# Performance work log

Measured on AMD Instinct MI355X. Metric: run time of the kernel, lower is better.

## Reference

```python
import jax, jax.numpy as jnp
import numpy as np

N, SD, VD, ED, E, NG, NA, NB = 512, 256, 128, 128, 262144, 16, 16, 5


def _lin_init(key, fan_in, fan_out):
    # torch.nn.Linear default: U(-1/sqrt(fan_in), 1/sqrt(fan_in)); stored as (in, out)
    lim = 1.0 / np.sqrt(fan_in)
    return jax.random.uniform(key, (fan_in, fan_out), jnp.float32, -lim, lim)


def setup_inputs() -> dict:
    key = jax.random.key(0)
    ks = jax.random.split(key, 20)
    s = jax.random.normal(ks[0], (N, SD), jnp.float32)
    v = jax.random.normal(ks[1], (N, 3, VD), jnp.float32)
    p = jax.random.normal(ks[2], (N, 3), jnp.float32)
    e = jax.random.normal(ks[3], (E, ED), jnp.float32)
    batch = jnp.sort(jax.random.randint(ks[4], (N,), 0, NG))
    edge_index_global = jax.random.randint(ks[5], (2, E), 0, N)
    W_sm = _lin_init(ks[6], SD, SD); b_sm = jnp.zeros((SD,), jnp.float32)
    W_bm = _lin_init(ks[7], ED, SD); b_bm = jnp.zeros((SD,), jnp.float32)
    W_b0 = _lin_init(ks[8], SD + 1, SD); b_b0 = jnp.zeros((SD,), jnp.float32)
    W_b1 = _lin_init(ks[9], SD, NB); b_b1 = jnp.zeros((NB,), jnp.float32)
    W_c = _lin_init(ks[10], VD, 1)  # no bias
    W_a = _lin_init(ks[11], SD, NA); b_a = jnp.zeros((NA,), jnp.float32)
    return {"s": s, "v": v, "p": p, "e": e, "batch": batch,
            "edge_index_global": edge_index_global,
            "W_sm": W_sm, "b_sm": b_sm, "W_bm": W_bm, "b_bm": b_bm,
            "W_b0": W_b0, "b_b0": b_b0, "W_b1": W_b1, "b_b1": b_b1,
            "W_c": W_c, "W_a": W_a, "b_a": b_a}


def reference(s, v, p, e, batch, edge_index_global,
              W_sm, b_sm, W_bm, b_bm, W_b0, b_b0, W_b1, b_b1, W_c, W_a, b_a):
    # shared_mapping: Linear + SiLU
    s = jax.nn.silu(s @ W_sm + b_sm)                      # [N, SD]
    coords_pred = (v @ W_c)[..., 0]                       # [N, 3]
    atoms_pred = s @ W_a + b_a                            # [N, NA]
    j, i = edge_index_global[0], edge_index_global[1]
    n = s.shape[0]
    # coords_param == 'data': coords = p + pred, then per-graph mean centering
    coords_pred = p + coords_pred
    seg_sum = jax.ops.segment_sum(coords_pred, batch, num_segments=NG)
    counts = jax.ops.segment_sum(jnp.ones((n, 1), coords_pred.dtype), batch, num_segments=NG)
    mean = seg_sum / jnp.maximum(counts, 1.0)
    coords_pred = coords_pred - mean[batch]
    # squared pairwise distance per edge
    d = jnp.sum((coords_pred[i] - coords_pred[j]) ** 2, axis=-1, keepdims=True)  # [E, 1]
    # sparse -> dense -> sparse symmetrization of edge features (as in the source)
    e_dense = jnp.zeros((n, n, e.shape[-1]), e.dtype).at[j, i].set(e)
    e_dense = 0.5 * (e_dense + jnp.transpose(e_dense, (1, 0, 2)))
    e_sym = e_dense[j, i]                                 # [E, ED]
    f = s[i] + s[j] + (e_sym @ W_bm + b_bm)               # [E, SD]
    edge = jnp.concatenate([f, d], axis=-1)               # [E, SD+1]
    bonds_pred = jax.nn.silu(edge @ W_b0 + b_b0) @ W_b1 + b_b1  # [E, NB]
    return coords_pred, atoms_pred, bonds_pred
```

## Files before the change

### kernel.cpp

```cpp
#include <hip/hip_runtime.h>
#include <math.h>

#define N_NODES 512
#define SD_ 256
#define VD_ 128
#define ED_ 128
#define NE_ 262144
#define NG_ 16
#define NA_ 16
#define NB_ 5
#define MAXP 131328

typedef __attribute__((ext_vector_type(8))) short bf16x8;
typedef __attribute__((ext_vector_type(4))) float f32x4;

__device__ __forceinline__ float silu_f(float x) { return x / (1.0f + expf(-x)); }
__device__ __forceinline__ float silu_fast(float x) {
    return x * __builtin_amdgcn_rcpf(1.0f + __builtin_amdgcn_exp2f(x * -1.44269504f));
}
__device__ __forceinline__ unsigned short f2bf(float x) {
    unsigned int u = __float_as_uint(x);
    return (unsigned short)((u + 0x7fffu + ((u >> 16) & 1u)) >> 16);
}
__device__ __forceinline__ float bf2f(unsigned short h) {
    return __uint_as_float(((unsigned int)h) << 16);
}
__device__ __forceinline__ unsigned int cvt_pk_bf16(float lo, float hi) {
    unsigned int r;
    asm("v_cvt_pk_bf16_f32 %0, %1, %2" : "=v"(r) : "v"(lo), "v"(hi));
    return r;
}

__device__ __forceinline__ void pack_one(
    const float* __restrict__ W, unsigned short* __restrict__ out, int nkb, int idx)
{
    int l = idx & 63;
    int kb = (idx >> 6) % nkb;
    int mtg = idx / (64 * nkb);
    int m = mtg * 16 + (l & 15);
    int k0 = kb * 32 + (l >> 4) * 8;
    bf16x8 pack;
    #pragma unroll
    for (int i = 0; i < 8; ++i) pack[i] = (short)f2bf(W[(size_t)(k0 + i) * SD_ + m]);
    *(bf16x8*)(out + (size_t)idx * 8) = pack;
}

__global__ __launch_bounds__(256) void prep_a(
    const int* __restrict__ ei, int* __restrict__ emap,
    const float* __restrict__ W_bm, const float* __restrict__ W_b0,
    unsigned short* __restrict__ WfA_bm, unsigned short* __restrict__ WfA_b0,
    const float* __restrict__ s, const float* __restrict__ v, const float* __restrict__ p,
    const float* __restrict__ W_sm, const float* __restrict__ b_sm,
    const float* __restrict__ W_a, const float* __restrict__ b_a,
    const float* __restrict__ W_c,
    unsigned short* __restrict__ s2b, float* __restrict__ cpred, float* __restrict__ atoms_out)
{
    __shared__ float srow[8][SD_];
    __shared__ float s2row[8][SD_];
    const int bid = blockIdx.x;
    const int tid = threadIdx.x;

    if (bid < 1024) {
        int k = bid * 256 + tid;
        int j = ei[k], i = ei[NE_ + k];
        atomicMax(&emap[j * N_NODES + i], k);
        return;
    }
    if (bid < 1072) {
        int idx = (bid - 1024) * 256 + tid;
        if (idx < 4096)  pack_one(W_bm, WfA_bm, 4, idx);
        else             pack_one(W_b0, WfA_b0, 8, idx - 4096);
        return;
    }
    if (bid < 1136) {
        const int n0 = (bid - 1072) * 8;
        #pragma unroll
        for (int n = 0; n < 8; ++n) srow[n][tid] = s[(size_t)(n0 + n) * SD_ + tid];
        __syncthreads();
        float acc[8];
        {
            float bb = b_sm[tid];
            #pragma unroll
            for (int n = 0; n < 8; ++n) acc[n] = bb;
        }
        #pragma unroll 4
        for (int c = 0; c < SD_; ++c) {
            float wv = W_sm[(size_t)c * SD_ + tid];
            #pragma unroll
            for (int n = 0; n < 8; ++n) acc[n] = fmaf(srow[n][c], wv, acc[n]);
        }
        #pragma unroll
        for (int n = 0; n < 8; ++n) {
            float sv = silu_f(acc[n]);
            s2b[(size_t)(n0 + n) * SD_ + tid] = f2bf(sv);
            s2row[n][tid] = sv;
        }
        __syncthreads();
        if (tid < 128) {
            int n = tid >> 4, a = tid & 15;
            float x = b_a[a];
            #pragma unroll 8
            for (int c = 0; c < SD_; ++c) x = fmaf(s2row[n][c], W_a[(size_t)c * NA_ + a], x);
            atoms_out[(size_t)(n0 + n) * NA_ + a] = x;
        }
        return;
    }
    for (int o = tid; o < N_NODES * 3; o += 256) {
        float x = p[o];
        const float* vr = v + (size_t)o * VD_;
        #pragma unroll 8
        for (int c = 0; c < VD_; ++c) x = fmaf(vr[c], W_c[c], x);
        cpred[o] = x;
    }
}

__global__ __launch_bounds__(512) void prep_b(
    const float* __restrict__ cpred, const int* __restrict__ batch,
    float* __restrict__ coords_ws, float* __restrict__ coords_out,
    const int* __restrict__ emap, int* __restrict__ counter,
    int* __restrict__ pairslot, int4* __restrict__ worklist)
{
    __shared__ float cl[N_NODES * 3];
    __shared__ int   bl[N_NODES];
    __shared__ float meanv[NG_ * 3];
    const int tid = threadIdx.x;

    if (blockIdx.x == 0) {
        bl[tid] = batch[tid];
        #pragma unroll
        for (int dd = 0; dd < 3; ++dd) cl[tid * 3 + dd] = cpred[tid * 3 + dd];
        __syncthreads();
        if (tid < NG_ * 3) {
            int g = tid / 3, dd = tid % 3;
            float sum = 0.f; int cnt = 0;
            for (int n = 0; n < N_NODES; ++n) {
                if (bl[n] == g) { sum += cl[n * 3 + dd]; cnt++; }
            }
            meanv[tid] = sum / (float)(cnt > 0 ? cnt : 1);
        }
        __syncthreads();
        int g = bl[tid];
        #pragma unroll
        for (int dd = 0; dd < 3; ++dd) {
            float val = cl[tid * 3 + dd] - meanv[g * 3 + dd];
            coords_ws[tid * 3 + dd]  = val;
            coords_out[tid * 3 + dd] = val;
        }
        return;
    }
    int idx = (blockIdx.x - 1) * 512 + tid;
    int a = idx >> 9, b = idx & (N_NODES - 1);
    if (a > b) return;
    int k1 = emap[(a << 9) | b];
    int k2 = emap[(b << 9) | a];
    if (k1 >= 0 || k2 >= 0) {
        int slot = atomicAdd(counter, 1);
        pairslot[(a << 9) | b] = slot;
        pairslot[(b << 9) | a] = slot;
        worklist[slot] = make_int4(a, b, k1, k2);
    }
}

__global__ __launch_bounds__(256) void bonds_scatter(
    const int* __restrict__ ei, const int* __restrict__ pairslot,
    const float* __restrict__ repval, float* __restrict__ bonds_out)
{
    int k = blockIdx.x * 256 + threadIdx.x;
    int j = ei[k], i = ei[NE_ + k];
    int slot = pairslot[(j << 9) | i];
    const float* rp = repval + (size_t)slot * NB_;
    #pragma unroll
    for (int b = 0; b < NB_; ++b)
        bonds_out[(size_t)k * NB_ + b] = rp[b];
}

__global__ __launch_bounds__(512) void edge_mfma(
    const float* __restrict__ e, const int4* __restrict__ worklist,
    const int* __restrict__ counter, const float* __restrict__ coords,
    const float* __restrict__ zrow, const unsigned short* __restrict__ s2b,
    const unsigned short* __restrict__ WfA_bm, const unsigned short* __restrict__ WfA_b0,
    const float* __restrict__ W_b1,
    const float* __restrict__ b_bm, const float* __restrict__ W_b0_last,
    const float* __restrict__ b_b0, const float* __restrict__ b_b1,
    float* __restrict__ repval)
{
    const int blk = blockIdx.x;
    const int cnt = counter[0];
    if (blk * 64 >= cnt) return;

    __shared__ __align__(16) char smem0[64 * 128 * 2];
    __shared__ __align__(16) unsigned short fd_lds[64 * 256];
    __shared__ unsigned short wb1t[NB_ * 256];
    __shared__ float dw[64];
    __shared__ int li_s[64], lj_s[64];

    unsigned short* esym_lds   = (unsigned short*)smem0;
    float*          bonds_part = (float*)smem0;

    const int tid = threadIdx.x;
    const int l   = tid & 63;
    const int w   = tid >> 6;
    const int eLo = l & 15;
    const int hi  = l >> 4;

    if (tid < 256) {
        const int eL = l;
        const int q  = w;
        int widx = min(blk * 64 + eL, cnt - 1);
        int4 wk = worklist[widx];
        const float* r1 = (wk.z >= 0) ? (e + (size_t)wk.z * ED_) : zrow;
        const float* r2 = (wk.w >= 0) ? (e + (size_t)wk.w * ED_) : zrow;
        const float4* p1 = (const float4*)(r1 + q * 32);
        const float4* p2 = (const float4*)(r2 + q * 32);
        float4 va[8], vb[8];
        #pragma unroll
        for (int t = 0; t < 8; ++t) va[t] = p1[t];
        #pragma unroll
        for (int t = 0; t < 8; ++t) vb[t] = p2[t];
        #pragma unroll
        for (int t = 0; t < 8; ++t) {
            va[t].x += vb[t].x; va[t].y += vb[t].y;
            va[t].z += vb[t].z; va[t].w += vb[t].w;
        }
        int ntB = eL >> 4, eLoB = eL & 15;
        #pragma unroll
        for (int h2 = 0; h2 < 4; ++h2) {
            float4 x0 = va[h2 * 2], x1 = va[h2 * 2 + 1];
            uint4 c;
            c.x = cvt_pk_bf16(0.5f * x0.x, 0.5f * x0.y);
            c.y = cvt_pk_bf16(0.5f * x0.z, 0.5f * x0.w);
            c.z = cvt_pk_bf16(0.5f * x1.x, 0.5f * x1.y);
            c.w = cvt_pk_bf16(0.5f * x1.z, 0.5f * x1.w);
            int chunk = (ntB * 4 + q) * 64 + h2 * 16 + eLoB;
            *(uint4*)(&esym_lds[chunk * 8]) = c;
        }
    } else {
        int t = tid - 256;
        #pragma unroll
        for (int b = 0; b < NB_; ++b)
            wb1t[b * 256 + t] = f2bf(W_b1[(size_t)t * NB_ + b]);
        if (t < 64) {
            int widx = min(blk * 64 + t, cnt - 1);
            int4 wk = worklist[widx];
            li_s[t] = wk.x; lj_s[t] = wk.y;
            float dx = coords[wk.x * 3 + 0] - coords[wk.y * 3 + 0];
            float dy = coords[wk.x * 3 + 1] - coords[wk.y * 3 + 1];
            float dz = coords[wk.x * 3 + 2] - coords[wk.y * 3 + 2];
            dw[t] = dx * dx + dy * dy + dz * dz;
        }
    }

    bf16x8 a1p[2];
    #pragma unroll
    for (int mt = 0; mt < 2; ++mt)
        a1p[mt] = *(const bf16x8*)(WfA_bm + ((size_t)(((w * 2 + mt) * 4 + 0) * 64 + l) * 8));

    __syncthreads();

    f32x4 acc[2][4];
    #pragma unroll
    for (int mt = 0; mt < 2; ++mt)
        #pragma unroll
        for (int nt = 0; nt < 4; ++nt) acc[mt][nt] = (f32x4){0.f, 0.f, 0.f, 0.f};

    #pragma unroll
    for (int kb = 0; kb < 4; ++kb) {
        bf16x8 af[2], bfg[4];
        #pragma unroll
        for (int mt = 0; mt < 2; ++mt)
            af[mt] = (kb == 0) ? a1p[mt]
                   : *(const bf16x8*)(WfA_bm + ((size_t)(((w * 2 + mt) * 4 + kb) * 64 + l) * 8));
        #pragma unroll
        for (int nt = 0; nt < 4; ++nt)
            bfg[nt] = *(const bf16x8*)(&esym_lds[(size_t)((nt * 4 + kb) * 64 + l) * 8]);
        __builtin_amdgcn_s_setprio(1);
        #pragma unroll
        for (int mt = 0; mt < 2; ++mt)
            #pragma unroll
            for (int nt = 0; nt < 4; ++nt)
                acc[mt][nt] = __builtin_amdgcn_mfma_f32_16x16x32_bf16(af[mt], bfg[nt], acc[mt][nt], 0, 0, 0);
        __builtin_amdgcn_s_setprio(0);
    }

    bf16x8 a2p[2];
    #pragma unroll
    for (int mt = 0; mt < 2; ++mt)
        a2p[mt] = *(const bf16x8*)(WfA_b0 + ((size_t)(((w * 2 + mt) * 8 + 0) * 64 + l) * 8));

    #pragma unroll
    for (int mt = 0; mt < 2; ++mt) {
        int m0 = w * 32 + mt * 16 + hi * 4;
        float4 bb = *(const float4*)(b_bm + m0);
        #pragma unroll
        for (int nt = 0; nt < 4; ++nt) {
            int edge = nt * 16 + eLo;
            int ni = li_s[edge], nj = lj_s[edge];
            ushort4 si = *(const ushort4*)(s2b + (size_t)ni * SD_ + m0);
            ushort4 sj = *(const ushort4*)(s2b + (size_t)nj * SD_ + m0);
            f32x4 r = acc[mt][nt];
            float f0 = r[0] + bf2f(si.x) + bf2f(sj.x) + bb.x;
            float f1 = r[1] + bf2f(si.y) + bf2f(sj.y) + bb.y;
            float f2 = r[2] + bf2f(si.z) + bf2f(sj.z) + bb.z;
            float f3 = r[3] + bf2f(si.w) + bf2f(sj.w) + bb.w;
            uint2 pk;
            pk.x = cvt_pk_bf16(f0, f1);
            pk.y = cvt_pk_bf16(f2, f3);
            int c16 = m0 >> 3;
            int byteo = (edge << 9) + ((c16 ^ (edge & 7)) << 4) + ((m0 & 7) << 1);
            *(uint2*)((char*)fd_lds + byteo) = pk;
        }
    }
    __syncthreads();

    #pragma unroll
    for (int mt = 0; mt < 2; ++mt) {
        int m0 = w * 32 + mt * 16 + hi * 4;
        float4 b0 = *(const float4*)(b_b0 + m0);
        float4 w2 = *(const float4*)(W_b0_last + m0);
        #pragma unroll
        for (int nt = 0; nt < 4; ++nt) {
            float dd = dw[nt * 16 + eLo];
            acc[mt][nt] = (f32x4){fmaf(dd, w2.x, b0.x), fmaf(dd, w2.y, b0.y),
                                  fmaf(dd, w2.z, b0.z), fmaf(dd, w2.w, b0.w)};
        }
    }
    #pragma unroll
    for (int kb = 0; kb < 8; ++kb) {
        bf16x8 af[2], bfg[4];
        #pragma unroll
        for (int mt = 0; mt < 2; ++mt)
            af[mt] = (kb == 0) ? a2p[mt]
                   : *(const bf16x8*)(WfA_b0 + ((size_t)(((w * 2 + mt) * 8 + kb) * 64 + l) * 8));
        #pragma unroll
        for (int nt = 0; nt < 4; ++nt) {
            int edge = nt * 16 + eLo;
            int c16 = (kb << 2) + hi;
            int byteo = (edge << 9) + ((c16 ^ (edge & 7)) << 4);
            bfg[nt] = *(const bf16x8*)((const char*)fd_lds + byteo);
        }
        __builtin_amdgcn_s_setprio(1);
        #pragma unroll
        for (int mt = 0; mt < 2; ++mt)
            #pragma unroll
            for (int nt = 0; nt < 4; ++nt)
                acc[mt][nt] = __builtin_amdgcn_mfma_f32_16x16x32_bf16(af[mt], bfg[nt], acc[mt][nt], 0, 0, 0);
        __builtin_amdgcn_s_setprio(0);
    }

    float pb[4][NB_];
    #pragma unroll
    for (int nt = 0; nt < 4; ++nt)
        #pragma unroll
        for (int b = 0; b < NB_; ++b) pb[nt][b] = 0.f;
    #pragma unroll
    for (int mt = 0; mt < 2; ++mt) {
        int m0 = w * 32 + mt * 16 + hi * 4;
        ushort4 wv[NB_];
        #pragma unroll
        for (int b = 0; b < NB_; ++b)
            wv[b] = *(const ushort4*)(wb1t + b * 256 + m0);
        #pragma unroll
        for (int nt = 0; nt < 4; ++nt) {
            f32x4 r = acc[mt][nt];
            float h0 = silu_fast(r[0]);
            float h1 = silu_fast(r[1]);
            float h2 = silu_fast(r[2]);
            float h3 = silu_fast(r[3]);
            #pragma unroll
            for (int b = 0; b < NB_; ++b) {
                float t = fmaf(h0, bf2f(wv[b].x), fmaf(h1, bf2f(wv[b].y),
                          fmaf(h2, bf2f(wv[b].z), h3 * bf2f(wv[b].w))));
                pb[nt][b] += t;
            }
        }
    }
    #pragma unroll
    for (int off = 16; off <= 32; off <<= 1)
        #pragma unroll
        for (int nt = 0; nt < 4; ++nt)
            #pragma unroll
            for (int b = 0; b < NB_; ++b)
                pb[nt][b] += __shfl_xor(pb[nt][b], off);

    __syncthreads();
    if (hi == 0) {
        #pragma unroll
        for (int nt = 0; nt < 4; ++nt)
            #pragma unroll
            for (int b = 0; b < NB_; ++b)
                bonds_part[(size_t)(w * 64 + nt * 16 + eLo) * NB_ + b] = pb[nt][b];
    }
    __syncthreads();

    for (int idx = tid; idx < 64 * NB_; idx += 512) {
        int edge = idx / NB_, b = idx % NB_;
        float s8 = 0.f;
        #pragma unroll
        for (int pp = 0; pp < 8; ++pp)
            s8 += bonds_part[(size_t)(pp * 64 + edge) * NB_ + b];
        repval[(size_t)(blk * 64 + edge) * NB_ + b] = s8 + b_b1[b];
    }
}

extern "C" void kernel_launch(void* const* d_in, const int* in_sizes, int n_in,
                              void* d_out, int out_size, void* d_ws, size_t ws_size,
                              hipStream_t stream)
{
    const float* s    = (const float*)d_in[0];
    const float* v    = (const float*)d_in[1];
    const float* p    = (const float*)d_in[2];
    const float* e    = (const float*)d_in[3];
    const int*   batch= (const int*)d_in[4];
    const int*   ei   = (const int*)d_in[5];
    const float* W_sm = (const float*)d_in[6];
    const float* b_sm = (const float*)d_in[7];
    const float* W_bm = (const float*)d_in[8];
    const float* b_bm = (const float*)d_in[9];
    const float* W_b0 = (const float*)d_in[10];
    const float* b_b0 = (const float*)d_in[11];
    const float* W_b1 = (const float*)d_in[12];
    const float* b_b1 = (const float*)d_in[13];
    const float* W_c  = (const float*)d_in[14];
    const float* W_a  = (const float*)d_in[15];
    const float* b_a  = (const float*)d_in[16];

    float* out = (float*)d_out;
    float* coords_out = out;
    float* atoms_out  = out + 1536;
    float* bonds_out  = out + 1536 + 8192;

    char* ws = (char*)d_ws;
    int*            emap    = (int*)ws;
    unsigned short* s2b     = (unsigned short*)(ws + 0x100000);
    unsigned short* WfA_bm  = (unsigned short*)(ws + 0x140000);
    unsigned short* WfA_b0  = (unsigned short*)(ws + 0x150000);
    float*          cpred   = (float*)(ws + 0x170000);
    float*          coords  = (float*)(ws + 0x172000);
    int*            counter = (int*)(ws + 0x175000);
    float*          zrow    = (float*)(ws + 0x175100);
    int*            pairslot= (int*)(ws + 0x180000);
    int4*           worklist= (int4*)(ws + 0x280000);
    float*          repval  = (float*)(ws + 0x4B0000);

    hipMemsetAsync(emap, 0xFF, N_NODES * N_NODES * sizeof(int), stream);
    hipMemsetAsync(ws + 0x175000, 0, 0x300, stream);

    prep_a<<<1137, 256, 0, stream>>>(ei, emap, W_bm, W_b0, WfA_bm, WfA_b0,
                                     s, v, p, W_sm, b_sm, W_a, b_a, W_c,
                                     s2b, cpred, atoms_out);
    prep_b<<<513, 512, 0, stream>>>(cpred, batch, coords, coords_out,
                                    emap, counter, pairslot, worklist);

    edge_mfma<<<(MAXP + 63) / 64, 512, 0, stream>>>(e, worklist, counter, coords, zrow, s2b,
                                                    WfA_bm, WfA_b0, W_b1,
                                                    b_bm, W_b0 + 256 * SD_, b_b0, b_b1,
                                                    repval);
    bonds_scatter<<<NE_ / 256, 256, 0, stream>>>(ei, pairslot, repval, bonds_out);
}
```

Measured before the change: 152.6 us.

## Spread node MLP over more blocks, fold memset into prep, flatten bond scatter

The shared-mapping node MLP now runs 2 nodes per block across 256 blocks instead of 8 nodes per block across 64, which raises parallelism at the cost of more W_sm re-reads. The counter/zrow memset is removed and the reset moves into the prep_a tail block, saving one API op. bonds_scatter now uses one thread per output element so stores coalesce, at the cost of recomputing the pairslot lookup five times per edge. edge_mfma prefetches all four W_bm A-fragments before the sync, which adds register pressure.

```diff
diff --git a/kernel.cpp b/kernel.cpp
--- a/kernel.cpp
+++ b/kernel.cpp
@@ -53,10 +53,11 @@
     const float* __restrict__ W_sm, const float* __restrict__ b_sm,
     const float* __restrict__ W_a, const float* __restrict__ b_a,
     const float* __restrict__ W_c,
-    unsigned short* __restrict__ s2b, float* __restrict__ cpred, float* __restrict__ atoms_out)
-{
-    __shared__ float srow[8][SD_];
-    __shared__ float s2row[8][SD_];
+    unsigned short* __restrict__ s2b, float* __restrict__ cpred, float* __restrict__ atoms_out,
+    int* __restrict__ counter, float* __restrict__ zrow)
+{
+    __shared__ float srow[2][SD_];
+    __shared__ float s2row[2][SD_];
     const int bid = blockIdx.x;
     const int tid = threadIdx.x;
 
@@ -72,31 +73,30 @@
         else             pack_one(W_b0, WfA_b0, 8, idx - 4096);
         return;
     }
-    if (bid < 1136) {
-        const int n0 = (bid - 1072) * 8;
-        #pragma unroll
-        for (int n = 0; n < 8; ++n) srow[n][tid] = s[(size_t)(n0 + n) * SD_ + tid];
+    if (bid < 1328) {
+        const int n0 = (bid - 1072) * 2;
+        #pragma unroll
+        for (int n = 0; n < 2; ++n) srow[n][tid] = s[(size_t)(n0 + n) * SD_ + tid];
         __syncthreads();
-        float acc[8];
+        float acc[2];
         {
             float bb = b_sm[tid];
-            #pragma unroll
-            for (int n = 0; n < 8; ++n) acc[n] = bb;
-        }
-        #pragma unroll 4
+            acc[0] = bb; acc[1] = bb;
+        }
+        #pragma unroll 8
         for (int c = 0; c < SD_; ++c) {
             float wv = W_sm[(size_t)c * SD_ + tid];
-            #pragma unroll
-            for (int n = 0; n < 8; ++n) acc[n] = fmaf(srow[n][c], wv, acc[n]);
-        }
-        #pragma unroll
-        for (int n = 0; n < 8; ++n) {
+            acc[0] = fmaf(srow[0][c], wv, acc[0]);
+            acc[1] = fmaf(srow[1][c], wv, acc[1]);
+        }
+        #pragma unroll
+        for (int n = 0; n < 2; ++n) {
             float sv = silu_f(acc[n]);
             s2b[(size_t)(n0 + n) * SD_ + tid] = f2bf(sv);
             s2row[n][tid] = sv;
         }
         __syncthreads();
-        if (tid < 128) {
+        if (tid < 32) {
             int n = tid >> 4, a = tid & 15;
             float x = b_a[a];
             #pragma unroll 8
@@ -105,6 +105,8 @@
         }
         return;
     }
+    if (tid == 0) counter[0] = 0;
+    if (tid < ED_) zrow[tid] = 0.0f;
     for (int o = tid; o < N_NODES * 3; o += 256) {
         float x = p[o];
         const float* vr = v + (size_t)o * VD_;
@@ -163,15 +165,15 @@
 
 __global__ __launch_bounds__(256) void bonds_scatter(
     const int* __restrict__ ei, const int* __restrict__ pairslot,
-    const float* __restrict__ repval, float* __restrict__ bonds_out)
-{
-    int k = blockIdx.x * 256 + threadIdx.x;
+    const float* __restrict__ repval, const float* __restrict__ b_b1,
+    float* __restrict__ bonds_out)
+{
+    int idx = blockIdx.x * 256 + threadIdx.x;
+    int k = idx / NB_;
+    int b = idx - k * NB_;
     int j = ei[k], i = ei[NE_ + k];
     int slot = pairslot[(j << 9) | i];
-    const float* rp = repval + (size_t)slot * NB_;
-    #pragma unroll
-    for (int b = 0; b < NB_; ++b)
-        bonds_out[(size_t)k * NB_ + b] = rp[b];
+    bonds_out[idx] = repval[(size_t)slot * NB_ + b];
 }
 
 __global__ __launch_bounds__(512) void edge_mfma(
@@ -202,6 +204,13 @@
     const int w   = tid >> 6;
     const int eLo = l & 15;
     const int hi  = l >> 4;
+
+    bf16x8 a1pf[4][2];
+    #pragma unroll
+    for (int kb = 0; kb < 4; ++kb)
+        #pragma unroll
+        for (int mt = 0; mt < 2; ++mt)
+            a1pf[kb][mt] = *(const bf16x8*)(WfA_bm + ((size_t)(((w * 2 + mt) * 4 + kb) * 64 + l) * 8));
 
     if (tid < 256) {
         const int eL = l;
@@ -250,26 +259,17 @@
         }
     }
 
-    bf16x8 a1p[2];
+    __syncthreads();
+
+    f32x4 acc[2][4];
     #pragma unroll
     for (int mt = 0; mt < 2; ++mt)
-        a1p[mt] = *(const bf16x8*)(WfA_bm + ((size_t)(((w * 2 + mt) * 4 + 0) * 64 + l) * 8));
-
-    __syncthreads();
-
-    f32x4 acc[2][4];
-    #pragma unroll
-    for (int mt = 0; mt < 2; ++mt)
         #pragma unroll
         for (int nt = 0; nt < 4; ++nt) acc[mt][nt] = (f32x4){0.f, 0.f, 0.f, 0.f};
 
     #pragma unroll
     for (int kb = 0; kb < 4; ++kb) {
-        bf16x8 af[2], bfg[4];
-        #pragma unroll
-        for (int mt = 0; mt < 2; ++mt)
-            af[mt] = (kb == 0) ? a1p[mt]
-                   : *(const bf16x8*)(WfA_bm + ((size_t)(((w * 2 + mt) * 4 + kb) * 64 + l) * 8));
+        bf16x8 bfg[4];
         #pragma unroll
         for (int nt = 0; nt < 4; ++nt)
             bfg[nt] = *(const bf16x8*)(&esym_lds[(size_t)((nt * 4 + kb) * 64 + l) * 8]);
@@ -278,7 +278,7 @@
         for (int mt = 0; mt < 2; ++mt)
             #pragma unroll
             for (int nt = 0; nt < 4; ++nt)
-                acc[mt][nt] = __builtin_amdgcn_mfma_f32_16x16x32_bf16(af[mt], bfg[nt], acc[mt][nt], 0, 0, 0);
+                acc[mt][nt] = __builtin_amdgcn_mfma_f32_16x16x32_bf16(a1pf[kb][mt], bfg[nt], acc[mt][nt], 0, 0, 0);
         __builtin_amdgcn_s_setprio(0);
     }
 
@@ -443,11 +443,10 @@
     float*          repval  = (float*)(ws + 0x4B0000);
 
     hipMemsetAsync(emap, 0xFF, N_NODES * N_NODES * sizeof(int), stream);
-    hipMemsetAsync(ws + 0x175000, 0, 0x300, stream);
-
-    prep_a<<<1137, 256, 0, stream>>>(ei, emap, W_bm, W_b0, WfA_bm, WfA_b0,
+
+    prep_a<<<1329, 256, 0, stream>>>(ei, emap, W_bm, W_b0, WfA_bm, WfA_b0,
                                      s, v, p, W_sm, b_sm, W_a, b_a, W_c,
-                                     s2b, cpred, atoms_out);
+                                     s2b, cpred, atoms_out, counter, zrow);
     prep_b<<<513, 512, 0, stream>>>(cpred, batch, coords, coords_out,
                                     emap, counter, pairslot, worklist);
 
@@ -455,5 +454,5 @@
                                                     WfA_bm, WfA_b0, W_b1,
                                                     b_bm, W_b0 + 256 * SD_, b_b0, b_b1,
                                                     repval);
-    bonds_scatter<<<NE_ / 256, 256, 0, stream>>>(ei, pairslot, repval, bonds_out);
-}
+    bonds_scatter<<<NE_ * NB_ / 256, 256, 0, stream>>>(ei, pairslot, repval, b_b1, bonds_out);
+}
```

Measured after the change: 151.4 us. Within noise of the previous version (-0.8%).
